# Optimization experiments

Hardware: AMD Instinct MI355X
Metric: run time of the kernel (lower is better)

Reference implementation:

```python
import jax, jax.numpy as jnp
import numpy as np

N_NODES = 50000
N_EDGES = 800000
D_IN, D_HID, D_ENC = 256, 128, 64


def setup_inputs() -> dict:
    key = jax.random.key(0)
    ks = jax.random.split(key, 8)
    x = jax.random.normal(ks[0], (N_NODES, D_IN), dtype=jnp.float32)
    edge_index = jax.random.randint(ks[1], (2, N_EDGES), 0, N_NODES, dtype=jnp.int64)
    # GCNConv params: lin weight (no bias) + separate bias, stored as [in, out]
    W1 = jax.random.normal(ks[2], (D_IN, D_HID), dtype=jnp.float32) * (1.0 / np.sqrt(D_IN))
    b1 = jnp.zeros((D_HID,), dtype=jnp.float32)
    W2 = jax.random.normal(ks[3], (D_HID, D_ENC), dtype=jnp.float32) * (1.0 / np.sqrt(D_HID))
    b2 = jnp.zeros((D_ENC,), dtype=jnp.float32)
    Wfc = jax.random.normal(ks[4], (D_ENC, 1), dtype=jnp.float32) * (1.0 / np.sqrt(D_ENC))
    bfc = jnp.zeros((1,), dtype=jnp.float32)
    return {"x": x, "edge_index": edge_index, "W1": W1, "b1": b1,
            "W2": W2, "b2": b2, "Wfc": Wfc, "bfc": bfc}


def gcn_conv(x, W, b, row, col, norm, n_nodes):
    """PyG GCNConv (normalize=True): D^-1/2 (A+I) D^-1/2 X W + b."""
    h = x @ W                                   # [N, out]
    msg = h[row] * norm[:, None]                # [E+N, out] gather + scale
    out = jax.ops.segment_sum(msg, col, num_segments=n_nodes)  # scatter-add
    return out + b


def gcn_norm(edge_index, n_nodes, dtype):
    loop = jnp.arange(n_nodes, dtype=edge_index.dtype)
    row = jnp.concatenate([edge_index[0], loop])  # sources
    col = jnp.concatenate([edge_index[1], loop])  # targets
    deg = jax.ops.segment_sum(jnp.ones_like(col, dtype=dtype), col,
                              num_segments=n_nodes)
    dinv = jnp.where(deg > 0, jax.lax.rsqrt(jnp.maximum(deg, 1e-12)), 0.0)
    norm = dinv[row] * dinv[col]
    return row, col, norm


def reference(x, edge_index, W1, b1, W2, b2, Wfc, bfc):
    n = x.shape[0]
    row, col, norm = gcn_norm(edge_index, n, x.dtype)
    h = gcn_conv(x, W1, b1, row, col, norm, n)
    h = jax.nn.relu(h)
    # dropout p=0 / eval mode: identity
    h = gcn_conv(h, W2, b2, row, col, norm, n)
    out = jax.nn.sigmoid(h @ Wfc + bfc)          # [N, 1]
    return out
```

## Files before the change

kernel.cpp:

```cpp
#include <hip/hip_runtime.h>
#include <hip/hip_bf16.h>
#include <cmath>

#define N_NODES 50000
#define N_EDGES 800000
#define D_IN 256
#define D_HID 128
#define D_ENC 64
#define NBUK 128
#define BSH 9
#define BMSK 511
#define BCAP 16384
#define PB_EPT 16
#define NCSRB 98
#define NGEMB 782

typedef short short8 __attribute__((ext_vector_type(8)));
typedef float floatx4 __attribute__((ext_vector_type(4)));
typedef float floatx8 __attribute__((ext_vector_type(8)));
typedef unsigned short ushort8v __attribute__((ext_vector_type(8)));

static __device__ __forceinline__ unsigned short f2bf(float f) {
    unsigned int u = __float_as_uint(f);
    unsigned int r = (u + 0x7FFFu + ((u >> 16) & 1u)) >> 16;
    return (unsigned short)r;
}
static __device__ __forceinline__ float bf2f(unsigned short u) {
    return __uint_as_float(((unsigned int)u) << 16);
}
static __device__ __forceinline__ floatx8 bf2f8(ushort8v u) {
    floatx8 f;
#pragma unroll
    for (int j = 0; j < 8; ++j) f[j] = bf2f(u[j]);
    return f;
}

static __device__ __forceinline__ void wswz(const float* __restrict__ W,
                                            unsigned short* __restrict__ Wsw,
                                            int t, int K, int N) {
    int KS = K / 32;
    int lane = t & 63;
    int ks   = (t >> 6) % KS;
    int ct   = (t >> 6) / KS;
    int m = lane & 15, quad = lane >> 4;
    int kbase = ks * 32 + quad * 8;
    int col   = ct * 16 + m;
#pragma unroll
    for (int j = 0; j < 8; ++j)
        Wsw[t * 8 + j] = f2bf(W[(size_t)(kbase + j) * N + col]);
}

__global__ __launch_bounds__(256) void part_k(const int* __restrict__ rows,
                                              const int* __restrict__ cols,
                                              int* __restrict__ bcur,
                                              unsigned int* __restrict__ brecs,
                                              const float* __restrict__ W1,
                                              const float* __restrict__ W2,
                                              const float* __restrict__ b2,
                                              const float* __restrict__ Wfc,
                                              unsigned short* __restrict__ Wsw1,
                                              float* __restrict__ w2fc,
                                              float* __restrict__ b2fc) {
    __shared__ unsigned int recs[256 * PB_EPT];
    __shared__ int h[NBUK], ex[NBUK], gbase[NBUK];
    int tid = threadIdx.x;
    int t = blockIdx.x * 256 + tid;
    if (t < 4096) wswz(W1, Wsw1, t, D_IN, D_HID);
    else if (t < 4224) {
        int c = t - 4096;
        float s = 0.0f;
#pragma unroll 8
        for (int j = 0; j < D_ENC; ++j) s += W2[c * D_ENC + j] * Wfc[j];
        w2fc[c] = s;
    } else if (t == 4224) {
        float s = 0.0f;
        for (int j = 0; j < D_ENC; ++j) s += b2[j] * Wfc[j];
        b2fc[0] = s;
    }

    if (tid < NBUK) h[tid] = 0;
    __syncthreads();
    int e0 = blockIdx.x * (256 * PB_EPT);
    unsigned int myrec[PB_EPT];
    int myb[PB_EPT];
#pragma unroll
    for (int j = 0; j < PB_EPT; ++j) {
        int e = e0 + j * 256 + tid;
        if (e < N_EDGES) {
            int s = rows[e], d = cols[e];
            myrec[j] = ((unsigned int)s << 16) | (unsigned int)d;
            myb[j] = d >> BSH;
            atomicAdd(&h[myb[j]], 1);
        } else myb[j] = -1;
    }
    __syncthreads();
    if (tid < NBUK) {
        int c = h[tid];
        gbase[tid] = tid * BCAP + (c ? atomicAdd(&bcur[tid], c) : 0);
        ex[tid] = c;
    }
    __syncthreads();
    for (int off = 1; off < NBUK; off <<= 1) {
        int v = 0;
        if (tid < NBUK && tid >= off) v = ex[tid - off];
        __syncthreads();
        if (tid < NBUK) ex[tid] += v;
        __syncthreads();
    }
    if (tid < NBUK) { ex[tid] -= h[tid]; h[tid] = 0; }
    __syncthreads();
#pragma unroll
    for (int j = 0; j < PB_EPT; ++j) {
        if (myb[j] >= 0) {
            int p = ex[myb[j]] + atomicAdd(&h[myb[j]], 1);
            recs[p] = myrec[j];
        }
    }
    __syncthreads();
    int w = tid >> 6, lane = tid & 63;
    for (int b = w; b < NBUK; b += 4) {
        int start = ex[b], cnt = h[b], gb = gbase[b];
        int lim = (b + 1) * BCAP;
        for (int i = lane; i < cnt; i += 64) {
            int gp = gb + i;
            if (gp < lim) brecs[gp] = recs[start + i];
        }
    }
}

__global__ __launch_bounds__(512) void csr_gemm_k(const unsigned int* __restrict__ brecs,
                                                  const int* __restrict__ bcur,
                                                  int* __restrict__ rowptr,
                                                  int* __restrict__ rowcnt,
                                                  unsigned short* __restrict__ srcs,
                                                  float* __restrict__ dinv,
                                                  const float4* __restrict__ X4,
                                                  const unsigned short* __restrict__ Wsw,
                                                  unsigned short* __restrict__ H) {
    extern __shared__ char dynsm[];
    int tid = threadIdx.x;
    if (blockIdx.x < NCSRB) {
        int* s   = (int*)dynsm;
        int* cur = (int*)(dynsm + 2048);
        unsigned short* sl = (unsigned short*)(dynsm + 4096);
        int b = blockIdx.x;
        int cb = bcur[b]; if (cb > BCAP) cb = BCAP;
        int ebeg = b * BCAP, eend = ebeg + cb;
        s[tid] = 0;
        __syncthreads();
        for (int e = ebeg + tid; e < eend; e += 512)
            atomicAdd(&s[brecs[e] & BMSK], 1);
        __syncthreads();
        int v = s[tid];
        for (int off = 1; off < 512; off <<= 1) {
            int t = (tid >= off) ? s[tid - off] : 0;
            __syncthreads();
            s[tid] += t;
            __syncthreads();
        }
        int excl = s[tid] - v;
        cur[tid] = excl;
        int node = (b << BSH) + tid;
        if (node < N_NODES) {
            rowptr[node] = ebeg + excl;
            rowcnt[node] = v;
            dinv[node] = rsqrtf((float)(v + 1));
        }
        __syncthreads();
        for (int e = ebeg + tid; e < eend; e += 512) {
            unsigned int rec = brecs[e];
            int p = atomicAdd(&cur[rec & BMSK], 1);
            sl[p] = (unsigned short)(rec >> 16);
        }
        __syncthreads();
        int nw = (cb + 1) >> 1;
        unsigned int* s32 = (unsigned int*)(srcs + ebeg);
        const unsigned int* l32 = (const unsigned int*)sl;
        for (int t = tid; t < nw; t += 512) s32[t] = l32[t];
    } else {
        constexpr int KP = D_IN + 8;
        unsigned short* As = (unsigned short*)dynsm;
        int row0 = (blockIdx.x - NCSRB) * 64;
        for (int idx = tid; idx < 64 * 64; idx += 512) {
            int r = idx >> 6, c4 = idx & 63;
            int gr = row0 + r;
            float4 v = (gr < N_NODES) ? X4[(size_t)gr * 64 + c4] : float4{0, 0, 0, 0};
            __hip_bfloat162 p0 = __float22bfloat162_rn(float2{v.x, v.y});
            __hip_bfloat162 p1 = __float22bfloat162_rn(float2{v.z, v.w});
            uint2 u; u.x = *(unsigned int*)&p0; u.y = *(unsigned int*)&p1;
            *(uint2*)&As[r * KP + c4 * 4] = u;
        }
        __syncthreads();

        int w    = tid >> 6;
        int lane = tid & 63;
        int m    = lane & 15;
        int quad = lane >> 4;
        int rsub = w & 3;
        int cth  = w >> 2;

        floatx4 acc[4];
#pragma unroll
        for (int ct = 0; ct < 4; ++ct)
#pragma unroll
            for (int i = 0; i < 4; ++i) acc[ct][i] = 0.0f;

#pragma unroll
        for (int ks = 0; ks < D_IN / 32; ++ks) {
            short8 af = *(const short8*)&As[(rsub * 16 + m) * KP + ks * 32 + quad * 8];
#pragma unroll
            for (int ct = 0; ct < 4; ++ct) {
                int ct4 = cth * 4 + ct;
                short8 bf = *(const short8*)&Wsw[(size_t)((ct4 * (D_IN / 32) + ks) * 64 + lane) * 8];
                acc[ct] = __builtin_amdgcn_mfma_f32_16x16x32_bf16(af, bf, acc[ct], 0, 0, 0);
            }
        }

        int rbase = row0 + rsub * 16 + quad * 4;
#pragma unroll
        for (int ct = 0; ct < 4; ++ct) {
            int col = (cth * 4 + ct) * 16 + m;
#pragma unroll
            for (int reg = 0; reg < 4; ++reg) {
                int r = rbase + reg;
                if (r < N_NODES) H[(size_t)r * D_HID + col] = f2bf(acc[ct][reg]);
            }
        }
    }
}

#define WGATHER(SP)                                                            \
    {                                                                          \
        const auto* sp_ = (SP);                                                \
        int i = 0;                                                             \
        for (; i + 8 <= cnt; i += 8) {                                         \
            int s0 = sp_[i],     s1 = sp_[i + 1], s2 = sp_[i + 2], s3 = sp_[i + 3]; \
            int s4 = sp_[i + 4], s5 = sp_[i + 5], s6 = sp_[i + 6], s7 = sp_[i + 7]; \
            float w0 = dinv[s0], w1 = dinv[s1], w2 = dinv[s2], w3 = dinv[s3];  \
            float w4 = dinv[s4], w5 = dinv[s5], w6 = dinv[s6], w7 = dinv[s7];  \
            ushort8v v0 = hs[(size_t)s0 * 16 + d8], v1 = hs[(size_t)s1 * 16 + d8]; \
            ushort8v v2 = hs[(size_t)s2 * 16 + d8], v3 = hs[(size_t)s3 * 16 + d8]; \
            ushort8v v4 = hs[(size_t)s4 * 16 + d8], v5 = hs[(size_t)s5 * 16 + d8]; \
            ushort8v v6 = hs[(size_t)s6 * 16 + d8], v7 = hs[(size_t)s7 * 16 + d8]; \
            a0 += bf2f8(v0) * w0; a1 += bf2f8(v1) * w1;                        \
            a2 += bf2f8(v2) * w2; a3 += bf2f8(v3) * w3;                        \
            a0 += bf2f8(v4) * w4; a1 += bf2f8(v5) * w5;                        \
            a2 += bf2f8(v6) * w6; a3 += bf2f8(v7) * w7;                        \
        }                                                                      \
        if (i + 4 <= cnt) {                                                    \
            int s0 = sp_[i], s1 = sp_[i + 1], s2 = sp_[i + 2], s3 = sp_[i + 3]; \
            a0 += bf2f8(hs[(size_t)s0 * 16 + d8]) * dinv[s0];                  \
            a1 += bf2f8(hs[(size_t)s1 * 16 + d8]) * dinv[s1];                  \
            a2 += bf2f8(hs[(size_t)s2 * 16 + d8]) * dinv[s2];                  \
            a3 += bf2f8(hs[(size_t)s3 * 16 + d8]) * dinv[s3];                  \
            i += 4;                                                            \
        }                                                                      \
        for (; i < cnt; ++i) {                                                 \
            int s = sp_[i];                                                    \
            a0 += bf2f8(hs[(size_t)s * 16 + d8]) * dinv[s];                    \
        }                                                                      \
    }

__global__ __launch_bounds__(256) void g1z_k(const ushort8v* __restrict__ hs,
                                             const int* __restrict__ rowptr,
                                             const int* __restrict__ rowcnt,
                                             const unsigned short* __restrict__ srcs,
                                             const float* __restrict__ dinv,
                                             const float4* __restrict__ b1_4,
                                             const float4* __restrict__ w2fc4,
                                             float* __restrict__ z) {
    __shared__ unsigned short sidx[1024];
    __shared__ int sb2[2];
    int tid = threadIdx.x;
    int nodeb = blockIdx.x * 16;
    int ln = tid >> 4;
    int d8 = tid & 15;
    int node = nodeb + ln;
    int beg = rowptr[node];
    int cnt = rowcnt[node];
    if (tid == 0)   sb2[0] = beg;
    if (tid == 240) sb2[1] = beg + cnt;
    ushort8v selfv = hs[(size_t)node * 16 + d8];
    float di = dinv[node];
    __syncthreads();
    int base = sb2[0], total = sb2[1] - base;
    for (int t = tid; t < total && t < 1024; t += 256) sidx[t] = srcs[base + t];
    __syncthreads();

    floatx8 a0 = {0,0,0,0,0,0,0,0}, a1 = a0, a2 = a0, a3 = a0;
    if (total <= 1024) {
        WGATHER(sidx + (beg - base))
    } else {
        WGATHER(srcs + beg)
    }
    floatx8 acc = a0 + a1 + a2 + a3 + bf2f8(selfv) * di;
    float4 bA = b1_4[d8 * 2],  bB = b1_4[d8 * 2 + 1];
    float4 wA = w2fc4[d8 * 2], wB = w2fc4[d8 * 2 + 1];
    float s = fmaxf(di * acc[0] + bA.x, 0.0f) * wA.x
            + fmaxf(di * acc[1] + bA.y, 0.0f) * wA.y
            + fmaxf(di * acc[2] + bA.z, 0.0f) * wA.z
            + fmaxf(di * acc[3] + bA.w, 0.0f) * wA.w
            + fmaxf(di * acc[4] + bB.x, 0.0f) * wB.x
            + fmaxf(di * acc[5] + bB.y, 0.0f) * wB.y
            + fmaxf(di * acc[6] + bB.z, 0.0f) * wB.z
            + fmaxf(di * acc[7] + bB.w, 0.0f) * wB.w;
#pragma unroll
    for (int off = 8; off; off >>= 1) s += __shfl_xor(s, off, 16);
    if (d8 == 0) z[node] = di * s;
}

__global__ __launch_bounds__(256) void gatherz_k(const float* __restrict__ z,
                                                 const int* __restrict__ rowptr,
                                                 const int* __restrict__ rowcnt,
                                                 const unsigned short* __restrict__ srcs,
                                                 const float* __restrict__ dinv,
                                                 const float* __restrict__ b2fc,
                                                 const float* __restrict__ bfc,
                                                 float* __restrict__ out) {
    int v = blockIdx.x * 256 + threadIdx.x;
    if (v >= N_NODES) return;
    int beg = rowptr[v], cnt = rowcnt[v];
    float s0 = z[v], s1 = 0.0f, s2 = 0.0f, s3 = 0.0f;
    int i = beg, end = beg + cnt;
    for (; i + 4 <= end; i += 4) {
        s0 += z[srcs[i]];
        s1 += z[srcs[i + 1]];
        s2 += z[srcs[i + 2]];
        s3 += z[srcs[i + 3]];
    }
    for (; i < end; ++i) s0 += z[srcs[i]];
    float p = dinv[v] * (s0 + s1 + s2 + s3) + b2fc[0] + bfc[0];
    out[v] = 1.0f / (1.0f + expf(-p));
}

extern "C" void kernel_launch(void* const* d_in, const int* in_sizes, int n_in,
                              void* d_out, int out_size, void* d_ws, size_t ws_size,
                              hipStream_t stream) {
    const float* x   = (const float*)d_in[0];
    const int*   ei  = (const int*)d_in[1];
    const float* W1  = (const float*)d_in[2];
    const float* b1  = (const float*)d_in[3];
    const float* W2  = (const float*)d_in[4];
    const float* b2  = (const float*)d_in[5];
    const float* Wfc = (const float*)d_in[6];
    const float* bfc = (const float*)d_in[7];
    float* out = (float*)d_out;

    const int* rows = ei;
    const int* cols = ei + N_EDGES;

    float* ws     = (float*)d_ws;
    float* dinv   = ws;
    int*   rowptr = (int*)(ws + 50048);
    int*   rowcnt = rowptr + 50048;
    int*   bcur   = rowcnt + 50048;
    unsigned int* brecs = (unsigned int*)(bcur + 128);
    unsigned short* srcs = (unsigned short*)(brecs + NBUK * BCAP);
    unsigned short* h1 = srcs + (size_t)NBUK * BCAP;
    unsigned short* Wsw1 = h1 + (size_t)N_NODES * D_HID;
    float* z    = (float*)(Wsw1 + (size_t)D_IN * D_HID);
    float* w2fc = z + 50000;
    float* b2fc = w2fc + 128;

    hipMemsetAsync(bcur, 0, NBUK * sizeof(int), stream);
    part_k<<<(N_EDGES + 256 * PB_EPT - 1) / (256 * PB_EPT), 256, 0, stream>>>(
        rows, cols, bcur, brecs, W1, W2, b2, Wfc, Wsw1, w2fc, b2fc);

    csr_gemm_k<<<NCSRB + NGEMB, 512, 36864, stream>>>(brecs, bcur, rowptr, rowcnt, srcs, dinv,
                                                      (const float4*)x, Wsw1, h1);

    g1z_k<<<N_NODES / 16, 256, 0, stream>>>((const ushort8v*)h1, rowptr, rowcnt, srcs, dinv,
                                            (const float4*)b1, (const float4*)w2fc, z);

    gatherz_k<<<(N_NODES + 255) / 256, 256, 0, stream>>>(z, rowptr, rowcnt, srcs, dinv,
                                                         b2fc, bfc, out);
}
```

Baseline: 164.9 us.

## Co-schedule edge partitioning with GEMM and split CSR build into its own kernel

Moves the weight swizzle and fc-weight folding into a small prep kernel that also zeroes the bucket counters, replacing the memset. Edge bucketing now runs in the same launch as the X·W1 GEMM blocks, with 196 blocks of 512 threads each handling 4096 edges. The per-bucket CSR build, which used to share a launch with the GEMM, becomes a separate kernel. The aim is to overlap the bandwidth-bound partition pass with the compute-bound GEMM instead of running them back to back; the price is still four dependent launches and the CSR build no longer hiding behind GEMM work.

```diff
diff --git a/kernel.cpp b/kernel.cpp
--- a/kernel.cpp
+++ b/kernel.cpp
@@ -11,8 +11,8 @@
 #define BSH 9
 #define BMSK 511
 #define BCAP 16384
-#define PB_EPT 16
-#define NCSRB 98
+#define PBF_EPT 8
+#define NPARTB 196
 #define NGEMB 782
 
 typedef short short8 __attribute__((ext_vector_type(8)));
@@ -50,21 +50,15 @@
         Wsw[t * 8 + j] = f2bf(W[(size_t)(kbase + j) * N + col]);
 }
 
-__global__ __launch_bounds__(256) void part_k(const int* __restrict__ rows,
-                                              const int* __restrict__ cols,
-                                              int* __restrict__ bcur,
-                                              unsigned int* __restrict__ brecs,
-                                              const float* __restrict__ W1,
+__global__ __launch_bounds__(256) void prep_k(const float* __restrict__ W1,
                                               const float* __restrict__ W2,
                                               const float* __restrict__ b2,
                                               const float* __restrict__ Wfc,
                                               unsigned short* __restrict__ Wsw1,
                                               float* __restrict__ w2fc,
-                                              float* __restrict__ b2fc) {
-    __shared__ unsigned int recs[256 * PB_EPT];
-    __shared__ int h[NBUK], ex[NBUK], gbase[NBUK];
-    int tid = threadIdx.x;
-    int t = blockIdx.x * 256 + tid;
+                                              float* __restrict__ b2fc,
+                                              int* __restrict__ bcur) {
+    int t = blockIdx.x * 256 + threadIdx.x;
     if (t < 4096) wswz(W1, Wsw1, t, D_IN, D_HID);
     else if (t < 4224) {
         int c = t - 4096;
@@ -76,111 +70,77 @@
         float s = 0.0f;
         for (int j = 0; j < D_ENC; ++j) s += b2[j] * Wfc[j];
         b2fc[0] = s;
-    }
-
-    if (tid < NBUK) h[tid] = 0;
-    __syncthreads();
-    int e0 = blockIdx.x * (256 * PB_EPT);
-    unsigned int myrec[PB_EPT];
-    int myb[PB_EPT];
-#pragma unroll
-    for (int j = 0; j < PB_EPT; ++j) {
-        int e = e0 + j * 256 + tid;
-        if (e < N_EDGES) {
-            int s = rows[e], d = cols[e];
-            myrec[j] = ((unsigned int)s << 16) | (unsigned int)d;
-            myb[j] = d >> BSH;
-            atomicAdd(&h[myb[j]], 1);
-        } else myb[j] = -1;
-    }
-    __syncthreads();
-    if (tid < NBUK) {
-        int c = h[tid];
-        gbase[tid] = tid * BCAP + (c ? atomicAdd(&bcur[tid], c) : 0);
-        ex[tid] = c;
-    }
-    __syncthreads();
-    for (int off = 1; off < NBUK; off <<= 1) {
-        int v = 0;
-        if (tid < NBUK && tid >= off) v = ex[tid - off];
-        __syncthreads();
-        if (tid < NBUK) ex[tid] += v;
-        __syncthreads();
-    }
-    if (tid < NBUK) { ex[tid] -= h[tid]; h[tid] = 0; }
-    __syncthreads();
-#pragma unroll
-    for (int j = 0; j < PB_EPT; ++j) {
-        if (myb[j] >= 0) {
-            int p = ex[myb[j]] + atomicAdd(&h[myb[j]], 1);
-            recs[p] = myrec[j];
-        }
-    }
-    __syncthreads();
-    int w = tid >> 6, lane = tid & 63;
-    for (int b = w; b < NBUK; b += 4) {
-        int start = ex[b], cnt = h[b], gb = gbase[b];
-        int lim = (b + 1) * BCAP;
-        for (int i = lane; i < cnt; i += 64) {
-            int gp = gb + i;
-            if (gp < lim) brecs[gp] = recs[start + i];
-        }
-    }
-}
-
-__global__ __launch_bounds__(512) void csr_gemm_k(const unsigned int* __restrict__ brecs,
-                                                  const int* __restrict__ bcur,
-                                                  int* __restrict__ rowptr,
-                                                  int* __restrict__ rowcnt,
-                                                  unsigned short* __restrict__ srcs,
-                                                  float* __restrict__ dinv,
+    } else if (t >= 4225 && t < 4225 + NBUK) {
+        bcur[t - 4225] = 0;
+    }
+}
+
+__global__ __launch_bounds__(512) void partgemm_k(const int* __restrict__ rows,
+                                                  const int* __restrict__ cols,
+                                                  int* __restrict__ bcur,
+                                                  unsigned int* __restrict__ brecs,
                                                   const float4* __restrict__ X4,
                                                   const unsigned short* __restrict__ Wsw,
                                                   unsigned short* __restrict__ H) {
     extern __shared__ char dynsm[];
     int tid = threadIdx.x;
-    if (blockIdx.x < NCSRB) {
-        int* s   = (int*)dynsm;
-        int* cur = (int*)(dynsm + 2048);
-        unsigned short* sl = (unsigned short*)(dynsm + 4096);
-        int b = blockIdx.x;
-        int cb = bcur[b]; if (cb > BCAP) cb = BCAP;
-        int ebeg = b * BCAP, eend = ebeg + cb;
-        s[tid] = 0;
-        __syncthreads();
-        for (int e = ebeg + tid; e < eend; e += 512)
-            atomicAdd(&s[brecs[e] & BMSK], 1);
-        __syncthreads();
-        int v = s[tid];
-        for (int off = 1; off < 512; off <<= 1) {
-            int t = (tid >= off) ? s[tid - off] : 0;
+    if (blockIdx.x < NPARTB) {
+        unsigned int* recs = (unsigned int*)dynsm;
+        int* h     = (int*)(dynsm + 16384);
+        int* ex    = h + NBUK;
+        int* gbase = ex + NBUK;
+        if (tid < NBUK) h[tid] = 0;
+        __syncthreads();
+        int e0 = blockIdx.x * 4096;
+        unsigned int myrec[PBF_EPT];
+        int myb[PBF_EPT];
+#pragma unroll
+        for (int j = 0; j < PBF_EPT; ++j) {
+            int e = e0 + j * 512 + tid;
+            if (e < N_EDGES) {
+                int s = rows[e], d = cols[e];
+                myrec[j] = ((unsigned int)s << 16) | (unsigned int)d;
+                myb[j] = d >> BSH;
+                atomicAdd(&h[myb[j]], 1);
+            } else myb[j] = -1;
+        }
+        __syncthreads();
+        if (tid < NBUK) {
+            int c = h[tid];
+            gbase[tid] = tid * BCAP + (c ? atomicAdd(&bcur[tid], c) : 0);
+            ex[tid] = c;
+        }
+        __syncthreads();
+        for (int off = 1; off < NBUK; off <<= 1) {
+            int v = 0;
+            if (tid < NBUK && tid >= off) v = ex[tid - off];
             __syncthreads();
-            s[tid] += t;
+            if (tid < NBUK) ex[tid] += v;
             __syncthreads();
         }
-        int excl = s[tid] - v;
-        cur[tid] = excl;
-        int node = (b << BSH) + tid;
-        if (node < N_NODES) {
-            rowptr[node] = ebeg + excl;
-            rowcnt[node] = v;
-            dinv[node] = rsqrtf((float)(v + 1));
-        }
-        __syncthreads();
-        for (int e = ebeg + tid; e < eend; e += 512) {
-            unsigned int rec = brecs[e];
-            int p = atomicAdd(&cur[rec & BMSK], 1);
-            sl[p] = (unsigned short)(rec >> 16);
-        }
-        __syncthreads();
-        int nw = (cb + 1) >> 1;
-        unsigned int* s32 = (unsigned int*)(srcs + ebeg);
-        const unsigned int* l32 = (const unsigned int*)sl;
-        for (int t = tid; t < nw; t += 512) s32[t] = l32[t];
+        if (tid < NBUK) { ex[tid] -= h[tid]; h[tid] = 0; }
+        __syncthreads();
+#pragma unroll
+        for (int j = 0; j < PBF_EPT; ++j) {
+            if (myb[j] >= 0) {
+                int p = ex[myb[j]] + atomicAdd(&h[myb[j]], 1);
+                recs[p] = myrec[j];
+            }
+        }
+        __syncthreads();
+        int w = tid >> 6, lane = tid & 63;
+        for (int b = w; b < NBUK; b += 8) {
+            int start = ex[b], cnt = h[b], gb = gbase[b];
+            int lim = (b + 1) * BCAP;
+            for (int i = lane; i < cnt; i += 64) {
+                int gp = gb + i;
+                if (gp < lim) brecs[gp] = recs[start + i];
+            }
+        }
     } else {
         constexpr int KP = D_IN + 8;
         unsigned short* As = (unsigned short*)dynsm;
-        int row0 = (blockIdx.x - NCSRB) * 64;
+        int row0 = (blockIdx.x - NPARTB) * 64;
         for (int idx = tid; idx < 64 * 64; idx += 512) {
             int r = idx >> 6, c4 = idx & 63;
             int gr = row0 + r;
@@ -227,6 +187,52 @@
             }
         }
     }
+}
+
+__global__ __launch_bounds__(512) void bucket_csr_k(const unsigned int* __restrict__ brecs,
+                                                    const int* __restrict__ bcur,
+                                                    int* __restrict__ rowptr,
+                                                    int* __restrict__ rowcnt,
+                                                    unsigned short* __restrict__ srcs,
+                                                    float* __restrict__ dinv) {
+    __shared__ int s[512];
+    __shared__ int cur[512];
+    __shared__ unsigned short sl[BCAP];
+    int b = blockIdx.x;
+    int cb = bcur[b]; if (cb > BCAP) cb = BCAP;
+    int ebeg = b * BCAP, eend = ebeg + cb;
+    int tid = threadIdx.x;
+    s[tid] = 0;
+    __syncthreads();
+    for (int e = ebeg + tid; e < eend; e += 512)
+        atomicAdd(&s[brecs[e] & BMSK], 1);
+    __syncthreads();
+    int v = s[tid];
+    for (int off = 1; off < 512; off <<= 1) {
+        int t = (tid >= off) ? s[tid - off] : 0;
+        __syncthreads();
+        s[tid] += t;
+        __syncthreads();
+    }
+    int excl = s[tid] - v;
+    cur[tid] = excl;
+    int node = (b << BSH) + tid;
+    if (node < N_NODES) {
+        rowptr[node] = ebeg + excl;
+        rowcnt[node] = v;
+        dinv[node] = rsqrtf((float)(v + 1));
+    }
+    __syncthreads();
+    for (int e = ebeg + tid; e < eend; e += 512) {
+        unsigned int rec = brecs[e];
+        int p = atomicAdd(&cur[rec & BMSK], 1);
+        sl[p] = (unsigned short)(rec >> 16);
+    }
+    __syncthreads();
+    int nw = (cb + 1) >> 1;
+    unsigned int* s32 = (unsigned int*)(srcs + ebeg);
+    const unsigned int* l32 = (const unsigned int*)sl;
+    for (int t = tid; t < nw; t += 512) s32[t] = l32[t];
 }
 
 #define WGATHER(SP)                                                            \
@@ -362,12 +368,12 @@
     float* w2fc = z + 50000;
     float* b2fc = w2fc + 128;
 
-    hipMemsetAsync(bcur, 0, NBUK * sizeof(int), stream);
-    part_k<<<(N_EDGES + 256 * PB_EPT - 1) / (256 * PB_EPT), 256, 0, stream>>>(
-        rows, cols, bcur, brecs, W1, W2, b2, Wfc, Wsw1, w2fc, b2fc);
-
-    csr_gemm_k<<<NCSRB + NGEMB, 512, 36864, stream>>>(brecs, bcur, rowptr, rowcnt, srcs, dinv,
-                                                      (const float4*)x, Wsw1, h1);
+    prep_k<<<18, 256, 0, stream>>>(W1, W2, b2, Wfc, Wsw1, w2fc, b2fc, bcur);
+
+    partgemm_k<<<NPARTB + NGEMB, 512, 36864, stream>>>(rows, cols, bcur, brecs,
+                                                       (const float4*)x, Wsw1, h1);
+
+    bucket_csr_k<<<(N_NODES + 511) / 512, 512, 0, stream>>>(brecs, bcur, rowptr, rowcnt, srcs, dinv);
 
     g1z_k<<<N_NODES / 16, 256, 0, stream>>>((const ushort8v*)h1, rowptr, rowcnt, srcs, dinv,
                                             (const float4*)b1, (const float4*)w2fc, z);
```

Result: faster. 161.2 us (-2.3%).

## Replace bucketed partition CSR build with global-atomic degree count and scatter

Applied to the files above, without the earlier changes.

The two-level bucket partition plus per-bucket LDS sort is replaced by a global atomic degree histogram, a per-512-node-block scan that writes rowptr and dinv, and a scatter pass that fills srcs using atomics on per-node cursors. The GEMM blocks are split in half and co-scheduled with the scan and scatter kernels, so the CSR build overlaps with the X·W1 matmul. This removes the intermediate brecs buffer and its extra pass. In exchange it relies on many contended global atomics, and the order of sources within a row becomes nondeterministic.

```diff
diff --git a/kernel.cpp b/kernel.cpp
--- a/kernel.cpp
+++ b/kernel.cpp
@@ -7,13 +7,14 @@
 #define D_IN 256
 #define D_HID 128
 #define D_ENC 64
-#define NBUK 128
-#define BSH 9
-#define BMSK 511
-#define BCAP 16384
-#define PB_EPT 16
-#define NCSRB 98
+#define NBUKS 98
+#define BCAPS 16384
+#define NPREPB 9
+#define NDEGB 196
 #define NGEMB 782
+#define NGEMB_A 391
+#define NGEMB_B 391
+#define DYN_LDS 33792
 
 typedef short short8 __attribute__((ext_vector_type(8)));
 typedef float floatx4 __attribute__((ext_vector_type(4)));
@@ -50,182 +51,149 @@
         Wsw[t * 8 + j] = f2bf(W[(size_t)(kbase + j) * N + col]);
 }
 
-__global__ __launch_bounds__(256) void part_k(const int* __restrict__ rows,
-                                              const int* __restrict__ cols,
-                                              int* __restrict__ bcur,
-                                              unsigned int* __restrict__ brecs,
-                                              const float* __restrict__ W1,
-                                              const float* __restrict__ W2,
-                                              const float* __restrict__ b2,
-                                              const float* __restrict__ Wfc,
-                                              unsigned short* __restrict__ Wsw1,
-                                              float* __restrict__ w2fc,
-                                              float* __restrict__ b2fc) {
-    __shared__ unsigned int recs[256 * PB_EPT];
-    __shared__ int h[NBUK], ex[NBUK], gbase[NBUK];
-    int tid = threadIdx.x;
-    int t = blockIdx.x * 256 + tid;
-    if (t < 4096) wswz(W1, Wsw1, t, D_IN, D_HID);
-    else if (t < 4224) {
-        int c = t - 4096;
-        float s = 0.0f;
+__global__ __launch_bounds__(512) void pd_k(const float* __restrict__ W1,
+                                            const float* __restrict__ W2,
+                                            const float* __restrict__ b2,
+                                            const float* __restrict__ Wfc,
+                                            unsigned short* __restrict__ Wsw1,
+                                            float* __restrict__ w2fc,
+                                            float* __restrict__ b2fc,
+                                            const int* __restrict__ cols,
+                                            int* __restrict__ rowcnt) {
+    int tid = threadIdx.x;
+    if (blockIdx.x < NPREPB) {
+        int t = blockIdx.x * 512 + tid;
+        if (t < 4096) wswz(W1, Wsw1, t, D_IN, D_HID);
+        else if (t < 4224) {
+            int c = t - 4096;
+            float s = 0.0f;
 #pragma unroll 8
-        for (int j = 0; j < D_ENC; ++j) s += W2[c * D_ENC + j] * Wfc[j];
-        w2fc[c] = s;
-    } else if (t == 4224) {
-        float s = 0.0f;
-        for (int j = 0; j < D_ENC; ++j) s += b2[j] * Wfc[j];
-        b2fc[0] = s;
-    }
-
-    if (tid < NBUK) h[tid] = 0;
+            for (int j = 0; j < D_ENC; ++j) s += W2[c * D_ENC + j] * Wfc[j];
+            w2fc[c] = s;
+        } else if (t == 4224) {
+            float s = 0.0f;
+            for (int j = 0; j < D_ENC; ++j) s += b2[j] * Wfc[j];
+            b2fc[0] = s;
+        }
+    } else {
+        int e0 = (blockIdx.x - NPREPB) * 4096;
+#pragma unroll
+        for (int j = 0; j < 8; ++j) {
+            int e = e0 + j * 512 + tid;
+            if (e < N_EDGES) atomicAdd(&rowcnt[cols[e]], 1);
+        }
+    }
+}
+
+static __device__ void gemm_path(char* dynsm, int row0,
+                                 const floatx4* X4, const unsigned short* Wsw,
+                                 unsigned short* H) {
+    constexpr int KP = D_IN + 8;
+    unsigned short* As = (unsigned short*)dynsm;
+    int tid = threadIdx.x;
+    for (int idx = tid; idx < 64 * 64; idx += 512) {
+        int r = idx >> 6, c4 = idx & 63;
+        int gr = row0 + r;
+        floatx4 v = (gr < N_NODES) ? X4[(size_t)gr * 64 + c4] : (floatx4){0, 0, 0, 0};
+        __hip_bfloat162 p0 = __float22bfloat162_rn(float2{v[0], v[1]});
+        __hip_bfloat162 p1 = __float22bfloat162_rn(float2{v[2], v[3]});
+        uint2 u; u.x = *(unsigned int*)&p0; u.y = *(unsigned int*)&p1;
+        *(uint2*)&As[r * KP + c4 * 4] = u;
+    }
     __syncthreads();
-    int e0 = blockIdx.x * (256 * PB_EPT);
-    unsigned int myrec[PB_EPT];
-    int myb[PB_EPT];
-#pragma unroll
-    for (int j = 0; j < PB_EPT; ++j) {
-        int e = e0 + j * 256 + tid;
-        if (e < N_EDGES) {
-            int s = rows[e], d = cols[e];
-            myrec[j] = ((unsigned int)s << 16) | (unsigned int)d;
-            myb[j] = d >> BSH;
-            atomicAdd(&h[myb[j]], 1);
-        } else myb[j] = -1;
-    }
-    __syncthreads();
-    if (tid < NBUK) {
-        int c = h[tid];
-        gbase[tid] = tid * BCAP + (c ? atomicAdd(&bcur[tid], c) : 0);
-        ex[tid] = c;
-    }
-    __syncthreads();
-    for (int off = 1; off < NBUK; off <<= 1) {
-        int v = 0;
-        if (tid < NBUK && tid >= off) v = ex[tid - off];
+
+    int w    = tid >> 6;
+    int lane = tid & 63;
+    int m    = lane & 15;
+    int quad = lane >> 4;
+    int rsub = w & 3;
+    int cth  = w >> 2;
+
+    floatx4 acc[4];
+#pragma unroll
+    for (int ct = 0; ct < 4; ++ct)
+#pragma unroll
+        for (int i = 0; i < 4; ++i) acc[ct][i] = 0.0f;
+
+#pragma unroll
+    for (int ks = 0; ks < D_IN / 32; ++ks) {
+        short8 af = *(const short8*)&As[(rsub * 16 + m) * KP + ks * 32 + quad * 8];
+#pragma unroll
+        for (int ct = 0; ct < 4; ++ct) {
+            int ct4 = cth * 4 + ct;
+            short8 bf = *(const short8*)&Wsw[(size_t)((ct4 * (D_IN / 32) + ks) * 64 + lane) * 8];
+            acc[ct] = __builtin_amdgcn_mfma_f32_16x16x32_bf16(af, bf, acc[ct], 0, 0, 0);
+        }
+    }
+
+    int rbase = row0 + rsub * 16 + quad * 4;
+#pragma unroll
+    for (int ct = 0; ct < 4; ++ct) {
+        int col = (cth * 4 + ct) * 16 + m;
+#pragma unroll
+        for (int reg = 0; reg < 4; ++reg) {
+            int r = rbase + reg;
+            if (r < N_NODES) H[(size_t)r * D_HID + col] = f2bf(acc[ct][reg]);
+        }
+    }
+}
+
+__global__ __launch_bounds__(512) void sg_k(const int* __restrict__ rowcnt,
+                                            int* __restrict__ rowptr,
+                                            int* __restrict__ gcur,
+                                            float* __restrict__ dinv,
+                                            const floatx4* __restrict__ X4,
+                                            const unsigned short* __restrict__ Wsw,
+                                            unsigned short* __restrict__ H) {
+    extern __shared__ char dynsm[];
+    int tid = threadIdx.x;
+    if (blockIdx.x < NBUKS) {
+        int* s = (int*)dynsm;
+        int b = blockIdx.x;
+        int node = (b << 9) + tid;
+        bool valid = node < N_NODES;
+        int cnt = valid ? rowcnt[node] : 0;
+        s[tid] = cnt;
         __syncthreads();
-        if (tid < NBUK) ex[tid] += v;
-        __syncthreads();
-    }
-    if (tid < NBUK) { ex[tid] -= h[tid]; h[tid] = 0; }
-    __syncthreads();
-#pragma unroll
-    for (int j = 0; j < PB_EPT; ++j) {
-        if (myb[j] >= 0) {
-            int p = ex[myb[j]] + atomicAdd(&h[myb[j]], 1);
-            recs[p] = myrec[j];
-        }
-    }
-    __syncthreads();
-    int w = tid >> 6, lane = tid & 63;
-    for (int b = w; b < NBUK; b += 4) {
-        int start = ex[b], cnt = h[b], gb = gbase[b];
-        int lim = (b + 1) * BCAP;
-        for (int i = lane; i < cnt; i += 64) {
-            int gp = gb + i;
-            if (gp < lim) brecs[gp] = recs[start + i];
-        }
-    }
-}
-
-__global__ __launch_bounds__(512) void csr_gemm_k(const unsigned int* __restrict__ brecs,
-                                                  const int* __restrict__ bcur,
-                                                  int* __restrict__ rowptr,
-                                                  int* __restrict__ rowcnt,
-                                                  unsigned short* __restrict__ srcs,
-                                                  float* __restrict__ dinv,
-                                                  const float4* __restrict__ X4,
-                                                  const unsigned short* __restrict__ Wsw,
-                                                  unsigned short* __restrict__ H) {
-    extern __shared__ char dynsm[];
-    int tid = threadIdx.x;
-    if (blockIdx.x < NCSRB) {
-        int* s   = (int*)dynsm;
-        int* cur = (int*)(dynsm + 2048);
-        unsigned short* sl = (unsigned short*)(dynsm + 4096);
-        int b = blockIdx.x;
-        int cb = bcur[b]; if (cb > BCAP) cb = BCAP;
-        int ebeg = b * BCAP, eend = ebeg + cb;
-        s[tid] = 0;
-        __syncthreads();
-        for (int e = ebeg + tid; e < eend; e += 512)
-            atomicAdd(&s[brecs[e] & BMSK], 1);
-        __syncthreads();
-        int v = s[tid];
         for (int off = 1; off < 512; off <<= 1) {
             int t = (tid >= off) ? s[tid - off] : 0;
             __syncthreads();
             s[tid] += t;
             __syncthreads();
         }
-        int excl = s[tid] - v;
-        cur[tid] = excl;
-        int node = (b << BSH) + tid;
-        if (node < N_NODES) {
-            rowptr[node] = ebeg + excl;
-            rowcnt[node] = v;
-            dinv[node] = rsqrtf((float)(v + 1));
-        }
-        __syncthreads();
-        for (int e = ebeg + tid; e < eend; e += 512) {
-            unsigned int rec = brecs[e];
-            int p = atomicAdd(&cur[rec & BMSK], 1);
-            sl[p] = (unsigned short)(rec >> 16);
-        }
-        __syncthreads();
-        int nw = (cb + 1) >> 1;
-        unsigned int* s32 = (unsigned int*)(srcs + ebeg);
-        const unsigned int* l32 = (const unsigned int*)sl;
-        for (int t = tid; t < nw; t += 512) s32[t] = l32[t];
+        if (valid) {
+            int rp = b * BCAPS + (s[tid] - cnt);
+            rowptr[node] = rp;
+            gcur[node]   = rp;
+            dinv[node]   = rsqrtf((float)(cnt + 1));
+        }
     } else {
-        constexpr int KP = D_IN + 8;
-        unsigned short* As = (unsigned short*)dynsm;
-        int row0 = (blockIdx.x - NCSRB) * 64;
-        for (int idx = tid; idx < 64 * 64; idx += 512) {
-            int r = idx >> 6, c4 = idx & 63;
-            int gr = row0 + r;
-            float4 v = (gr < N_NODES) ? X4[(size_t)gr * 64 + c4] : float4{0, 0, 0, 0};
-            __hip_bfloat162 p0 = __float22bfloat162_rn(float2{v.x, v.y});
-            __hip_bfloat162 p1 = __float22bfloat162_rn(float2{v.z, v.w});
-            uint2 u; u.x = *(unsigned int*)&p0; u.y = *(unsigned int*)&p1;
-            *(uint2*)&As[r * KP + c4 * 4] = u;
-        }
-        __syncthreads();
-
-        int w    = tid >> 6;
-        int lane = tid & 63;
-        int m    = lane & 15;
-        int quad = lane >> 4;
-        int rsub = w & 3;
-        int cth  = w >> 2;
-
-        floatx4 acc[4];
-#pragma unroll
-        for (int ct = 0; ct < 4; ++ct)
-#pragma unroll
-            for (int i = 0; i < 4; ++i) acc[ct][i] = 0.0f;
-
-#pragma unroll
-        for (int ks = 0; ks < D_IN / 32; ++ks) {
-            short8 af = *(const short8*)&As[(rsub * 16 + m) * KP + ks * 32 + quad * 8];
-#pragma unroll
-            for (int ct = 0; ct < 4; ++ct) {
-                int ct4 = cth * 4 + ct;
-                short8 bf = *(const short8*)&Wsw[(size_t)((ct4 * (D_IN / 32) + ks) * 64 + lane) * 8];
-                acc[ct] = __builtin_amdgcn_mfma_f32_16x16x32_bf16(af, bf, acc[ct], 0, 0, 0);
+        gemm_path(dynsm, (blockIdx.x - NBUKS) * 64, X4, Wsw, H);
+    }
+}
+
+__global__ __launch_bounds__(512) void cg_k(const int* __restrict__ rows,
+                                            const int* __restrict__ cols,
+                                            int* __restrict__ gcur,
+                                            unsigned short* __restrict__ srcs,
+                                            const floatx4* __restrict__ X4,
+                                            const unsigned short* __restrict__ Wsw,
+                                            unsigned short* __restrict__ H) {
+    extern __shared__ char dynsm[];
+    int tid = threadIdx.x;
+    if (blockIdx.x < NDEGB) {
+        int e0 = blockIdx.x * 4096;
+#pragma unroll
+        for (int j = 0; j < 8; ++j) {
+            int e = e0 + j * 512 + tid;
+            if (e < N_EDGES) {
+                int s = rows[e], d = cols[e];
+                int p = atomicAdd(&gcur[d], 1);
+                srcs[p] = (unsigned short)s;
             }
         }
-
-        int rbase = row0 + rsub * 16 + quad * 4;
-#pragma unroll
-        for (int ct = 0; ct < 4; ++ct) {
-            int col = (cth * 4 + ct) * 16 + m;
-#pragma unroll
-            for (int reg = 0; reg < 4; ++reg) {
-                int r = rbase + reg;
-                if (r < N_NODES) H[(size_t)r * D_HID + col] = f2bf(acc[ct][reg]);
-            }
-        }
+    } else {
+        gemm_path(dynsm, (NGEMB_A + blockIdx.x - NDEGB) * 64, X4, Wsw, H);
     }
 }
 
@@ -353,21 +321,24 @@
     float* dinv   = ws;
     int*   rowptr = (int*)(ws + 50048);
     int*   rowcnt = rowptr + 50048;
-    int*   bcur   = rowcnt + 50048;
-    unsigned int* brecs = (unsigned int*)(bcur + 128);
-    unsigned short* srcs = (unsigned short*)(brecs + NBUK * BCAP);
-    unsigned short* h1 = srcs + (size_t)NBUK * BCAP;
+    int*   gcur   = rowcnt + 50048;
+    unsigned short* srcs = (unsigned short*)(gcur + 50048);
+    unsigned short* h1 = srcs + (size_t)NBUKS * BCAPS;
     unsigned short* Wsw1 = h1 + (size_t)N_NODES * D_HID;
     float* z    = (float*)(Wsw1 + (size_t)D_IN * D_HID);
     float* w2fc = z + 50000;
     float* b2fc = w2fc + 128;
 
-    hipMemsetAsync(bcur, 0, NBUK * sizeof(int), stream);
-    part_k<<<(N_EDGES + 256 * PB_EPT - 1) / (256 * PB_EPT), 256, 0, stream>>>(
-        rows, cols, bcur, brecs, W1, W2, b2, Wfc, Wsw1, w2fc, b2fc);
-
-    csr_gemm_k<<<NCSRB + NGEMB, 512, 36864, stream>>>(brecs, bcur, rowptr, rowcnt, srcs, dinv,
-                                                      (const float4*)x, Wsw1, h1);
+    hipMemsetAsync(rowcnt, 0, 50048 * sizeof(int), stream);
+
+    pd_k<<<NPREPB + NDEGB, 512, 0, stream>>>(W1, W2, b2, Wfc, Wsw1, w2fc, b2fc,
+                                             cols, rowcnt);
+
+    sg_k<<<NBUKS + NGEMB_A, 512, DYN_LDS, stream>>>(rowcnt, rowptr, gcur, dinv,
+                                                    (const floatx4*)x, Wsw1, h1);
+
+    cg_k<<<NDEGB + NGEMB_B, 512, DYN_LDS, stream>>>(rows, cols, gcur, srcs,
+                                                    (const floatx4*)x, Wsw1, h1);
 
     g1z_k<<<N_NODES / 16, 256, 0, stream>>>((const ushort8v*)h1, rowptr, rowcnt, srcs, dinv,
                                             (const float4*)b1, (const float4*)w2fc, z);
```

After: 218.8 us. 1.33x slower.

## Replace atomic bucket cursors with fixed per-block chunk slots and count table

Applied to the files above, without the earlier changes.

The edge partition no longer reserves space in each bucket through global atomics on a shared cursor array, so the memset of that array goes away. Each partition block writes up to 128 records into its own fixed slot per bucket and records the count in a table. The CSR builder scans all 196 slots of its bucket, using the counts to skip empty entries. The partition step now uses 196 blocks of 512 threads, and the weight prep moves into 9 extra blocks of the same kernel. In exchange the CSR pass reads padded slots, and any bucket that gets more than 128 edges from one block silently drops the extra edges.

```diff
diff --git a/kernel.cpp b/kernel.cpp
--- a/kernel.cpp
+++ b/kernel.cpp
@@ -10,10 +10,15 @@
 #define NBUK 128
 #define BSH 9
 #define BMSK 511
-#define BCAP 16384
-#define PB_EPT 16
 #define NCSRB 98
+#define NPARTB 196
+#define NPREPB 9
+#define CHUNK 128
+#define BCAPB (NPARTB * CHUNK)
+#define SCAP 16384
 #define NGEMB 782
+#define LDS_PP 17408
+#define LDS_GC 37376
 
 typedef short short8 __attribute__((ext_vector_type(8)));
 typedef float floatx4 __attribute__((ext_vector_type(4)));
@@ -50,42 +55,21 @@
         Wsw[t * 8 + j] = f2bf(W[(size_t)(kbase + j) * N + col]);
 }
 
-__global__ __launch_bounds__(256) void part_k(const int* __restrict__ rows,
-                                              const int* __restrict__ cols,
-                                              int* __restrict__ bcur,
-                                              unsigned int* __restrict__ brecs,
-                                              const float* __restrict__ W1,
-                                              const float* __restrict__ W2,
-                                              const float* __restrict__ b2,
-                                              const float* __restrict__ Wfc,
-                                              unsigned short* __restrict__ Wsw1,
-                                              float* __restrict__ w2fc,
-                                              float* __restrict__ b2fc) {
-    __shared__ unsigned int recs[256 * PB_EPT];
-    __shared__ int h[NBUK], ex[NBUK], gbase[NBUK];
+static __device__ void part_path(char* dynsm, int pb,
+                                 const int* rows, const int* cols,
+                                 unsigned int* brecs, unsigned short* cnts) {
+    unsigned int* recs = (unsigned int*)dynsm;
+    int* h  = (int*)(dynsm + 16384);
+    int* ex = h + NBUK;
     int tid = threadIdx.x;
-    int t = blockIdx.x * 256 + tid;
-    if (t < 4096) wswz(W1, Wsw1, t, D_IN, D_HID);
-    else if (t < 4224) {
-        int c = t - 4096;
-        float s = 0.0f;
-#pragma unroll 8
-        for (int j = 0; j < D_ENC; ++j) s += W2[c * D_ENC + j] * Wfc[j];
-        w2fc[c] = s;
-    } else if (t == 4224) {
-        float s = 0.0f;
-        for (int j = 0; j < D_ENC; ++j) s += b2[j] * Wfc[j];
-        b2fc[0] = s;
-    }
-
     if (tid < NBUK) h[tid] = 0;
     __syncthreads();
-    int e0 = blockIdx.x * (256 * PB_EPT);
-    unsigned int myrec[PB_EPT];
-    int myb[PB_EPT];
-#pragma unroll
-    for (int j = 0; j < PB_EPT; ++j) {
-        int e = e0 + j * 256 + tid;
+    int e0 = pb * 4096;
+    unsigned int myrec[8];
+    int myb[8];
+#pragma unroll
+    for (int j = 0; j < 8; ++j) {
+        int e = e0 + j * 512 + tid;
         if (e < N_EDGES) {
             int s = rows[e], d = cols[e];
             myrec[j] = ((unsigned int)s << 16) | (unsigned int)d;
@@ -94,11 +78,7 @@
         } else myb[j] = -1;
     }
     __syncthreads();
-    if (tid < NBUK) {
-        int c = h[tid];
-        gbase[tid] = tid * BCAP + (c ? atomicAdd(&bcur[tid], c) : 0);
-        ex[tid] = c;
-    }
+    if (tid < NBUK) ex[tid] = h[tid];
     __syncthreads();
     for (int off = 1; off < NBUK; off <<= 1) {
         int v = 0;
@@ -110,7 +90,7 @@
     if (tid < NBUK) { ex[tid] -= h[tid]; h[tid] = 0; }
     __syncthreads();
 #pragma unroll
-    for (int j = 0; j < PB_EPT; ++j) {
+    for (int j = 0; j < 8; ++j) {
         if (myb[j] >= 0) {
             int p = ex[myb[j]] + atomicAdd(&h[myb[j]], 1);
             recs[p] = myrec[j];
@@ -118,115 +98,167 @@
     }
     __syncthreads();
     int w = tid >> 6, lane = tid & 63;
-    for (int b = w; b < NBUK; b += 4) {
-        int start = ex[b], cnt = h[b], gb = gbase[b];
-        int lim = (b + 1) * BCAP;
-        for (int i = lane; i < cnt; i += 64) {
-            int gp = gb + i;
-            if (gp < lim) brecs[gp] = recs[start + i];
-        }
-    }
-}
-
-__global__ __launch_bounds__(512) void csr_gemm_k(const unsigned int* __restrict__ brecs,
-                                                  const int* __restrict__ bcur,
-                                                  int* __restrict__ rowptr,
-                                                  int* __restrict__ rowcnt,
-                                                  unsigned short* __restrict__ srcs,
-                                                  float* __restrict__ dinv,
-                                                  const float4* __restrict__ X4,
-                                                  const unsigned short* __restrict__ Wsw,
-                                                  unsigned short* __restrict__ H) {
+    for (int b = w; b < NBUK; b += 8) {
+        int start = ex[b], c = h[b];
+        int cw = c < CHUNK ? c : CHUNK;
+        if (lane == 0) cnts[b * NPARTB + pb] = (unsigned short)cw;
+        if (b < NCSRB) {
+            unsigned int gb = (unsigned int)b * BCAPB + pb * CHUNK;
+            for (int i = lane; i < cw; i += 64)
+                brecs[gb + i] = recs[start + i];
+        }
+    }
+}
+
+__global__ __launch_bounds__(512) void pp_k(const float* __restrict__ W1,
+                                            const float* __restrict__ W2,
+                                            const float* __restrict__ b2,
+                                            const float* __restrict__ Wfc,
+                                            unsigned short* __restrict__ Wsw1,
+                                            float* __restrict__ w2fc,
+                                            float* __restrict__ b2fc,
+                                            const int* __restrict__ rows,
+                                            const int* __restrict__ cols,
+                                            unsigned int* __restrict__ brecs,
+                                            unsigned short* __restrict__ cnts) {
     extern __shared__ char dynsm[];
     int tid = threadIdx.x;
-    if (blockIdx.x < NCSRB) {
-        int* s   = (int*)dynsm;
-        int* cur = (int*)(dynsm + 2048);
-        unsigned short* sl = (unsigned short*)(dynsm + 4096);
-        int b = blockIdx.x;
-        int cb = bcur[b]; if (cb > BCAP) cb = BCAP;
-        int ebeg = b * BCAP, eend = ebeg + cb;
-        s[tid] = 0;
+    if (blockIdx.x < NPREPB) {
+        int t = blockIdx.x * 512 + tid;
+        if (t < 4096) wswz(W1, Wsw1, t, D_IN, D_HID);
+        else if (t < 4224) {
+            int c = t - 4096;
+            float s = 0.0f;
+#pragma unroll 8
+            for (int j = 0; j < D_ENC; ++j) s += W2[c * D_ENC + j] * Wfc[j];
+            w2fc[c] = s;
+        } else if (t == 4224) {
+            float s = 0.0f;
+            for (int j = 0; j < D_ENC; ++j) s += b2[j] * Wfc[j];
+            b2fc[0] = s;
+        }
+    } else {
+        part_path(dynsm, blockIdx.x - NPREPB, rows, cols, brecs, cnts);
+    }
+}
+
+static __device__ void csr_path(char* dynsm, int b,
+                                const unsigned int* brecs, const unsigned short* cnts,
+                                int* rowptr, int* rowcnt,
+                                unsigned short* srcs, float* dinv) {
+    int* s   = (int*)dynsm;
+    int* cur = (int*)(dynsm + 2048);
+    unsigned short* sl = (unsigned short*)(dynsm + 4096);
+    unsigned short* scnt = (unsigned short*)(dynsm + 36864);
+    int tid = threadIdx.x;
+    if (tid < NPARTB) scnt[tid] = cnts[b * NPARTB + tid];
+    s[tid] = 0;
+    __syncthreads();
+    const unsigned int* bb = brecs + (size_t)b * BCAPB;
+    for (int idx = tid; idx < (NPARTB << 7); idx += 512) {
+        int pb = idx >> 7, i = idx & (CHUNK - 1);
+        if (i < (int)scnt[pb]) atomicAdd(&s[bb[idx] & BMSK], 1);
+    }
+    __syncthreads();
+    int v = s[tid];
+    for (int off = 1; off < 512; off <<= 1) {
+        int t = (tid >= off) ? s[tid - off] : 0;
         __syncthreads();
-        for (int e = ebeg + tid; e < eend; e += 512)
-            atomicAdd(&s[brecs[e] & BMSK], 1);
+        s[tid] += t;
         __syncthreads();
-        int v = s[tid];
-        for (int off = 1; off < 512; off <<= 1) {
-            int t = (tid >= off) ? s[tid - off] : 0;
-            __syncthreads();
-            s[tid] += t;
-            __syncthreads();
-        }
-        int excl = s[tid] - v;
-        cur[tid] = excl;
-        int node = (b << BSH) + tid;
-        if (node < N_NODES) {
-            rowptr[node] = ebeg + excl;
-            rowcnt[node] = v;
-            dinv[node] = rsqrtf((float)(v + 1));
-        }
-        __syncthreads();
-        for (int e = ebeg + tid; e < eend; e += 512) {
-            unsigned int rec = brecs[e];
+    }
+    int excl = s[tid] - v;
+    cur[tid] = excl;
+    int total = s[511];
+    int node = (b << BSH) + tid;
+    if (node < N_NODES) {
+        rowptr[node] = b * SCAP + excl;
+        rowcnt[node] = v;
+        dinv[node] = rsqrtf((float)(v + 1));
+    }
+    __syncthreads();
+    for (int idx = tid; idx < (NPARTB << 7); idx += 512) {
+        int pb = idx >> 7, i = idx & (CHUNK - 1);
+        if (i < (int)scnt[pb]) {
+            unsigned int rec = bb[idx];
             int p = atomicAdd(&cur[rec & BMSK], 1);
             sl[p] = (unsigned short)(rec >> 16);
         }
-        __syncthreads();
-        int nw = (cb + 1) >> 1;
-        unsigned int* s32 = (unsigned int*)(srcs + ebeg);
-        const unsigned int* l32 = (const unsigned int*)sl;
-        for (int t = tid; t < nw; t += 512) s32[t] = l32[t];
-    } else {
-        constexpr int KP = D_IN + 8;
-        unsigned short* As = (unsigned short*)dynsm;
-        int row0 = (blockIdx.x - NCSRB) * 64;
-        for (int idx = tid; idx < 64 * 64; idx += 512) {
-            int r = idx >> 6, c4 = idx & 63;
-            int gr = row0 + r;
-            float4 v = (gr < N_NODES) ? X4[(size_t)gr * 64 + c4] : float4{0, 0, 0, 0};
-            __hip_bfloat162 p0 = __float22bfloat162_rn(float2{v.x, v.y});
-            __hip_bfloat162 p1 = __float22bfloat162_rn(float2{v.z, v.w});
-            uint2 u; u.x = *(unsigned int*)&p0; u.y = *(unsigned int*)&p1;
-            *(uint2*)&As[r * KP + c4 * 4] = u;
-        }
-        __syncthreads();
-
-        int w    = tid >> 6;
-        int lane = tid & 63;
-        int m    = lane & 15;
-        int quad = lane >> 4;
-        int rsub = w & 3;
-        int cth  = w >> 2;
-
-        floatx4 acc[4];
-#pragma unroll
-        for (int ct = 0; ct < 4; ++ct)
-#pragma unroll
-            for (int i = 0; i < 4; ++i) acc[ct][i] = 0.0f;
-
-#pragma unroll
-        for (int ks = 0; ks < D_IN / 32; ++ks) {
-            short8 af = *(const short8*)&As[(rsub * 16 + m) * KP + ks * 32 + quad * 8];
-#pragma unroll
-            for (int ct = 0; ct < 4; ++ct) {
-                int ct4 = cth * 4 + ct;
-                short8 bf = *(const short8*)&Wsw[(size_t)((ct4 * (D_IN / 32) + ks) * 64 + lane) * 8];
-                acc[ct] = __builtin_amdgcn_mfma_f32_16x16x32_bf16(af, bf, acc[ct], 0, 0, 0);
-            }
-        }
-
-        int rbase = row0 + rsub * 16 + quad * 4;
+    }
+    __syncthreads();
+    int nw = (total + 1) >> 1;
+    unsigned int* s32 = (unsigned int*)(srcs + b * SCAP);
+    const unsigned int* l32 = (const unsigned int*)sl;
+    for (int t = tid; t < nw; t += 512) s32[t] = l32[t];
+}
+
+static __device__ void gemm_path(char* dynsm, int row0,
+                                 const floatx4* X4, const unsigned short* Wsw,
+                                 unsigned short* H) {
+    constexpr int KP = D_IN + 8;
+    unsigned short* As = (unsigned short*)dynsm;
+    int tid = threadIdx.x;
+    for (int idx = tid; idx < 64 * 64; idx += 512) {
+        int r = idx >> 6, c4 = idx & 63;
+        int gr = row0 + r;
+        floatx4 v = (gr < N_NODES) ? X4[(size_t)gr * 64 + c4] : (floatx4){0, 0, 0, 0};
+        __hip_bfloat162 p0 = __float22bfloat162_rn(float2{v[0], v[1]});
+        __hip_bfloat162 p1 = __float22bfloat162_rn(float2{v[2], v[3]});
+        uint2 u; u.x = *(unsigned int*)&p0; u.y = *(unsigned int*)&p1;
+        *(uint2*)&As[r * KP + c4 * 4] = u;
+    }
+    __syncthreads();
+
+    int w    = tid >> 6;
+    int lane = tid & 63;
+    int m    = lane & 15;
+    int quad = lane >> 4;
+    int rsub = w & 3;
+    int cth  = w >> 2;
+
+    floatx4 acc[4];
+#pragma unroll
+    for (int ct = 0; ct < 4; ++ct)
+#pragma unroll
+        for (int i = 0; i < 4; ++i) acc[ct][i] = 0.0f;
+
+#pragma unroll
+    for (int ks = 0; ks < D_IN / 32; ++ks) {
+        short8 af = *(const short8*)&As[(rsub * 16 + m) * KP + ks * 32 + quad * 8];
 #pragma unroll
         for (int ct = 0; ct < 4; ++ct) {
-            int col = (cth * 4 + ct) * 16 + m;
-#pragma unroll
-            for (int reg = 0; reg < 4; ++reg) {
-                int r = rbase + reg;
-                if (r < N_NODES) H[(size_t)r * D_HID + col] = f2bf(acc[ct][reg]);
-            }
-        }
-    }
+            int ct4 = cth * 4 + ct;
+            short8 bf = *(const short8*)&Wsw[(size_t)((ct4 * (D_IN / 32) + ks) * 64 + lane) * 8];
+            acc[ct] = __builtin_amdgcn_mfma_f32_16x16x32_bf16(af, bf, acc[ct], 0, 0, 0);
+        }
+    }
+
+    int rbase = row0 + rsub * 16 + quad * 4;
+#pragma unroll
+    for (int ct = 0; ct < 4; ++ct) {
+        int col = (cth * 4 + ct) * 16 + m;
+#pragma unroll
+        for (int reg = 0; reg < 4; ++reg) {
+            int r = rbase + reg;
+            if (r < N_NODES) H[(size_t)r * D_HID + col] = f2bf(acc[ct][reg]);
+        }
+    }
+}
+
+__global__ __launch_bounds__(512) void gc_k(const unsigned int* __restrict__ brecs,
+                                            const unsigned short* __restrict__ cnts,
+                                            int* __restrict__ rowptr,
+                                            int* __restrict__ rowcnt,
+                                            unsigned short* __restrict__ srcs,
+                                            float* __restrict__ dinv,
+                                            const floatx4* __restrict__ X4,
+                                            const unsigned short* __restrict__ Wsw,
+                                            unsigned short* __restrict__ H) {
+    extern __shared__ char dynsm[];
+    if (blockIdx.x < NCSRB)
+        csr_path(dynsm, blockIdx.x, brecs, cnts, rowptr, rowcnt, srcs, dinv);
+    else
+        gemm_path(dynsm, (blockIdx.x - NCSRB) * 64, X4, Wsw, H);
 }
 
 #define WGATHER(SP)                                                            \
@@ -353,21 +385,20 @@
     float* dinv   = ws;
     int*   rowptr = (int*)(ws + 50048);
     int*   rowcnt = rowptr + 50048;
-    int*   bcur   = rowcnt + 50048;
-    unsigned int* brecs = (unsigned int*)(bcur + 128);
-    unsigned short* srcs = (unsigned short*)(brecs + NBUK * BCAP);
-    unsigned short* h1 = srcs + (size_t)NBUK * BCAP;
+    unsigned short* cnts = (unsigned short*)(rowcnt + 50048);
+    unsigned int*   brecs = (unsigned int*)(cnts + NBUK * NPARTB);
+    unsigned short* srcs = (unsigned short*)(brecs + (size_t)NCSRB * BCAPB);
+    unsigned short* h1 = srcs + (size_t)NCSRB * SCAP;
     unsigned short* Wsw1 = h1 + (size_t)N_NODES * D_HID;
     float* z    = (float*)(Wsw1 + (size_t)D_IN * D_HID);
     float* w2fc = z + 50000;
     float* b2fc = w2fc + 128;
 
-    hipMemsetAsync(bcur, 0, NBUK * sizeof(int), stream);
-    part_k<<<(N_EDGES + 256 * PB_EPT - 1) / (256 * PB_EPT), 256, 0, stream>>>(
-        rows, cols, bcur, brecs, W1, W2, b2, Wfc, Wsw1, w2fc, b2fc);
-
-    csr_gemm_k<<<NCSRB + NGEMB, 512, 36864, stream>>>(brecs, bcur, rowptr, rowcnt, srcs, dinv,
-                                                      (const float4*)x, Wsw1, h1);
+    pp_k<<<NPREPB + NPARTB, 512, LDS_PP, stream>>>(W1, W2, b2, Wfc, Wsw1, w2fc, b2fc,
+                                                   rows, cols, brecs, cnts);
+
+    gc_k<<<NCSRB + NGEMB, 512, LDS_GC, stream>>>(brecs, cnts, rowptr, rowcnt, srcs, dinv,
+                                                 (const floatx4*)x, Wsw1, h1);
 
     g1z_k<<<N_NODES / 16, 256, 0, stream>>>((const ushort8v*)h1, rowptr, rowcnt, srcs, dinv,
                                             (const float4*)b1, (const float4*)w2fc, z);
```

Result: no change. 167.9 us (+1.8%).
